# Optimization experiments

Hardware: AMD Instinct MI355X
Metric: run time of the kernel (lower is better)

Reference implementation:

```python
import jax, jax.numpy as jnp
import numpy as np

B, C, W, H, X, Y = 8, 32, 256, 128, 720, 361


def setup_inputs() -> dict:
    key = jax.random.key(0)
    k1, k2, k3, k4, k5 = jax.random.split(key, 5)
    return {
        "wt": jax.random.normal(k1, (B, C, W, H), dtype=jnp.float32),
        "x_in_lon": jax.random.uniform(k2, (B, W), dtype=jnp.float32),
        "x_in_lat": jax.random.uniform(k3, (B, H), dtype=jnp.float32),
        "x_out_lon": jax.random.uniform(k4, (B, X), dtype=jnp.float32),
        "x_out_lat": jax.random.uniform(k5, (B, Y), dtype=jnp.float32),
        "init_ls": jnp.full((1,), 0.5, dtype=jnp.float32),
    }


def _rbf_weights(x1, x2, init_ls):
    # x1: [B,N], x2: [B,M] -> RBF weights [B,N,M]
    a = x1[..., None]  # [B,N,1]
    b = x2[..., None]  # [B,M,1]
    d2 = (jnp.sum(a * a, -1)[..., :, None]
          + jnp.sum(b * b, -1)[..., None, :]
          - 2.0 * jnp.einsum('bnk,bmk->bnm', a, b))
    return jnp.exp(-0.5 * d2 / (init_ls ** 2))


def reference(wt, x_in_lon, x_in_lat, x_out_lon, x_out_lat, init_ls):
    # density channel: 1 where wt channel 0 is finite, 0 where NaN
    density = jnp.where(jnp.isnan(wt[:, 0:1]), 0.0, 1.0)
    wt = jnp.concatenate([density, wt], axis=1)          # [B,C+1,W,H]
    wt = jnp.where(jnp.isnan(wt), 0.0, wt)
    w0 = _rbf_weights(x_in_lon, x_out_lon, init_ls[0])   # [B,W,X]
    w1 = _rbf_weights(x_in_lat, x_out_lat, init_ls[0])   # [B,H,Y]
    ee = jnp.einsum('bcwh,bwx,bhy->bcxy', wt, w0, w1)    # [B,C+1,X,Y]
    dens = ee[:, 0:1]
    out = jnp.concatenate(
        [dens, ee[:, 1:] / jnp.clip(dens, 1e-6, 1e5)], axis=1)
    return out
```

## Files before the change

kernel.cpp:

```cpp
#include <hip/hip_runtime.h>

#define NB 8
#define NC 32
#define NCP 33
#define NW 256
#define NH 128
#define NX 720
#define NY 361

typedef __attribute__((ext_vector_type(8))) short  short8;
typedef __attribute__((ext_vector_type(4))) float  f32x4;

static __device__ __forceinline__ unsigned short f2bf(float f) {
    union { float f; unsigned int u; } v; v.f = f;
    unsigned int r = (v.u + 0x7FFFu + ((v.u >> 16) & 1u)) >> 16;
    return (unsigned short)r;
}

__global__ __launch_bounds__(256) void rbf_w0_kernel(
    const float* __restrict__ lon_in, const float* __restrict__ lon_out,
    const float* __restrict__ ls, unsigned short* __restrict__ w0t)
{
    int idx = blockIdx.x * 256 + threadIdx.x;
    int w = idx & (NW - 1);
    int r = idx >> 8;
    int x = r % NX;
    int b = r / NX;
    float l = ls[0];
    float inv = -0.5f / (l * l);
    float d = lon_in[b * NW + w] - lon_out[b * NX + x];
    w0t[idx] = f2bf(__expf(inv * d * d));
}

__global__ __launch_bounds__(256) void rbf_w1_kernel(
    const float* __restrict__ lat_in, const float* __restrict__ lat_out,
    const float* __restrict__ ls, unsigned short* __restrict__ w1t)
{
    int idx = blockIdx.x * 256 + threadIdx.x;
    int h = idx & (NH - 1);
    int r = idx >> 7;
    int y = r % NY;
    int b = r / NY;
    float l = ls[0];
    float inv = -0.5f / (l * l);
    float d = lat_in[b * NH + h] - lat_out[b * NY + y];
    w1t[idx] = f2bf(__expf(inv * d * d));
}

__global__ __launch_bounds__(256) void prep_wtT_kernel(
    const float* __restrict__ wt, unsigned short* __restrict__ wtT)
{
    __shared__ float tile[64 * 129];
    const int bc = blockIdx.z;
    const int b = bc / NCP;
    const int c = bc - b * NCP;
    const int w0 = blockIdx.x * 64;
    const bool dens = (c == 0);
    const float* src = wt + ((size_t)b * NC + (dens ? 0 : (c - 1))) * (NW * NH);

    const int r4 = threadIdx.x >> 5;
    const int c4 = threadIdx.x & 31;
    #pragma unroll
    for (int p = 0; p < 8; ++p) {
        int r = r4 + p * 8;
        float4 v = *(const float4*)&src[(size_t)(w0 + r) * NH + c4 * 4];
        float o0 = (v.x != v.x) ? 0.f : (dens ? 1.f : v.x);
        float o1 = (v.y != v.y) ? 0.f : (dens ? 1.f : v.y);
        float o2 = (v.z != v.z) ? 0.f : (dens ? 1.f : v.z);
        float o3 = (v.w != v.w) ? 0.f : (dens ? 1.f : v.w);
        float* tp = &tile[r * 129 + c4 * 4];
        tp[0] = o0; tp[1] = o1; tp[2] = o2; tp[3] = o3;
    }
    __syncthreads();

    unsigned short* dst = wtT + (size_t)bc * (NH * NW);
    #pragma unroll
    for (int p = 0; p < 4; ++p) {
        int ch = threadIdx.x + p * 256;
        int wc = ch & 7;
        int h  = ch >> 3;
        unsigned int u[4];
        #pragma unroll
        for (int j = 0; j < 4; ++j) {
            unsigned int lo = f2bf(tile[(wc * 8 + 2 * j    ) * 129 + h]);
            unsigned int hi = f2bf(tile[(wc * 8 + 2 * j + 1) * 129 + h]);
            u[j] = lo | (hi << 16);
        }
        uint4 q = make_uint4(u[0], u[1], u[2], u[3]);
        *(uint4*)&dst[(size_t)h * NW + w0 + wc * 8] = q;
    }
}

__global__ __launch_bounds__(256) void stage1_mfma(
    const unsigned short* __restrict__ w0t,
    const unsigned short* __restrict__ wtT,
    unsigned short* __restrict__ t)
{
    __shared__ __align__(16) unsigned short As[64 * 88];
    __shared__ __align__(16) unsigned short Bs[64 * 88];

    const int bc = blockIdx.z;
    const int b  = bc / NCP;
    const int x0 = blockIdx.x * 64;
    const int h0 = blockIdx.y * 64;
    const int tid  = threadIdx.x;
    const int lane = tid & 63;
    const int wv   = tid >> 6;
    const int q    = lane >> 4;
    const int ln   = lane & 15;
    const int mw   = (wv & 1) * 32;
    const int nw   = (wv >> 1) * 32;

    const unsigned short* Ap = w0t + (size_t)b * NX * NW;
    const unsigned short* Bp = wtT + (size_t)bc * NH * NW;

    f32x4 acc[2][2];
    #pragma unroll
    for (int i = 0; i < 2; ++i)
        #pragma unroll
        for (int j = 0; j < 2; ++j)
            acc[i][j] = (f32x4){0.f, 0.f, 0.f, 0.f};

    const int r_ld  = tid >> 3;
    const int cc_ld = tid & 7;

    for (int k0 = 0; k0 < NW; k0 += 64) {
        #pragma unroll
        for (int p = 0; p < 2; ++p) {
            int r = r_ld + p * 32;
            int xr = x0 + r; if (xr > NX - 1) xr = NX - 1;
            *(uint4*)&As[r * 88 + cc_ld * 8] =
                *(const uint4*)&Ap[(size_t)xr * NW + k0 + cc_ld * 8];
            *(uint4*)&Bs[r * 88 + cc_ld * 8] =
                *(const uint4*)&Bp[(size_t)(h0 + r) * NW + k0 + cc_ld * 8];
        }
        __syncthreads();
        #pragma unroll
        for (int ki = 0; ki < 2; ++ki) {
            const int ko = ki * 32 + q * 8;
            short8 a0 = *(const short8*)&As[(mw      + ln) * 88 + ko];
            short8 a1 = *(const short8*)&As[(mw + 16 + ln) * 88 + ko];
            short8 b0 = *(const short8*)&Bs[(nw      + ln) * 88 + ko];
            short8 b1 = *(const short8*)&Bs[(nw + 16 + ln) * 88 + ko];
            acc[0][0] = __builtin_amdgcn_mfma_f32_16x16x32_bf16(a0, b0, acc[0][0], 0, 0, 0);
            acc[0][1] = __builtin_amdgcn_mfma_f32_16x16x32_bf16(a0, b1, acc[0][1], 0, 0, 0);
            acc[1][0] = __builtin_amdgcn_mfma_f32_16x16x32_bf16(a1, b0, acc[1][0], 0, 0, 0);
            acc[1][1] = __builtin_amdgcn_mfma_f32_16x16x32_bf16(a1, b1, acc[1][1], 0, 0, 0);
        }
        __syncthreads();
    }

    unsigned short* Cp = t + (size_t)bc * NX * NH;
    #pragma unroll
    for (int mi = 0; mi < 2; ++mi)
        #pragma unroll
        for (int reg = 0; reg < 4; ++reg) {
            int x = x0 + mw + mi * 16 + q * 4 + reg;
            if (x < NX) {
                size_t rowo = (size_t)x * NH;
                #pragma unroll
                for (int ni = 0; ni < 2; ++ni) {
                    int h = h0 + nw + ni * 16 + ln;
                    Cp[rowo + h] = f2bf(acc[mi][ni][reg]);
                }
            }
        }
}

template <bool DIV>
__global__ __launch_bounds__(256) void stage2_mfma(
    const unsigned short* __restrict__ t,
    const unsigned short* __restrict__ w1t,
    float* __restrict__ out)
{
    __shared__ __align__(16) unsigned short As[64 * 88];
    __shared__ __align__(16) unsigned short Bs[64 * 88];

    int b, c;
    if (DIV) { b = blockIdx.z >> 5; c = 1 + (blockIdx.z & 31); }
    else     { b = blockIdx.z;      c = 0; }
    const int bc = b * NCP + c;
    const int x0 = blockIdx.x * 64;
    const int y0 = blockIdx.y * 64;
    const int tid  = threadIdx.x;
    const int lane = tid & 63;
    const int wv   = tid >> 6;
    const int q    = lane >> 4;
    const int ln   = lane & 15;
    const int mw   = (wv & 1) * 32;
    const int nw   = (wv >> 1) * 32;

    const unsigned short* Ap = t + (size_t)bc * NX * NH;
    const unsigned short* Bp = w1t + (size_t)b * NY * NH;

    f32x4 acc[2][2];
    #pragma unroll
    for (int i = 0; i < 2; ++i)
        #pragma unroll
        for (int j = 0; j < 2; ++j)
            acc[i][j] = (f32x4){0.f, 0.f, 0.f, 0.f};

    const int r_ld  = tid >> 3;
    const int cc_ld = tid & 7;

    for (int k0 = 0; k0 < NH; k0 += 64) {
        #pragma unroll
        for (int p = 0; p < 2; ++p) {
            int r = r_ld + p * 32;
            int xr = x0 + r; if (xr > NX - 1) xr = NX - 1;
            int yr = y0 + r; if (yr > NY - 1) yr = NY - 1;
            *(uint4*)&As[r * 88 + cc_ld * 8] =
                *(const uint4*)&Ap[(size_t)xr * NH + k0 + cc_ld * 8];
            *(uint4*)&Bs[r * 88 + cc_ld * 8] =
                *(const uint4*)&Bp[(size_t)yr * NH + k0 + cc_ld * 8];
        }
        __syncthreads();
        #pragma unroll
        for (int ki = 0; ki < 2; ++ki) {
            const int ko = ki * 32 + q * 8;
            short8 a0 = *(const short8*)&As[(mw      + ln) * 88 + ko];
            short8 a1 = *(const short8*)&As[(mw + 16 + ln) * 88 + ko];
            short8 b0 = *(const short8*)&Bs[(nw      + ln) * 88 + ko];
            short8 b1 = *(const short8*)&Bs[(nw + 16 + ln) * 88 + ko];
            acc[0][0] = __builtin_amdgcn_mfma_f32_16x16x32_bf16(a0, b0, acc[0][0], 0, 0, 0);
            acc[0][1] = __builtin_amdgcn_mfma_f32_16x16x32_bf16(a0, b1, acc[0][1], 0, 0, 0);
            acc[1][0] = __builtin_amdgcn_mfma_f32_16x16x32_bf16(a1, b0, acc[1][0], 0, 0, 0);
            acc[1][1] = __builtin_amdgcn_mfma_f32_16x16x32_bf16(a1, b1, acc[1][1], 0, 0, 0);
        }
        __syncthreads();
    }

    const size_t plane = (size_t)NX * NY;
    float* Cp = out + (size_t)bc * plane;
    const float* Dp = out + (size_t)(b * NCP) * plane;

    #pragma unroll
    for (int mi = 0; mi < 2; ++mi)
        #pragma unroll
        for (int reg = 0; reg < 4; ++reg) {
            int x = x0 + mw + mi * 16 + q * 4 + reg;
            if (x < NX) {
                size_t rowo = (size_t)x * NY;
                #pragma unroll
                for (int ni = 0; ni < 2; ++ni) {
                    int y = y0 + nw + ni * 16 + ln;
                    if (y < NY) {
                        float val = acc[mi][ni][reg];
                        if (DIV) {
                            float dv = Dp[rowo + y];
                            dv = fminf(fmaxf(dv, 1e-6f), 1e5f);
                            val /= dv;
                        }
                        Cp[rowo + y] = val;
                    }
                }
            }
        }
}

extern "C" void kernel_launch(void* const* d_in, const int* in_sizes, int n_in,
                              void* d_out, int out_size, void* d_ws, size_t ws_size,
                              hipStream_t stream)
{
    const float* wt      = (const float*)d_in[0];
    const float* lon_in  = (const float*)d_in[1];
    const float* lat_in  = (const float*)d_in[2];
    const float* lon_out = (const float*)d_in[3];
    const float* lat_out = (const float*)d_in[4];
    const float* ls      = (const float*)d_in[5];
    float* out = (float*)d_out;

    unsigned short* w0t = (unsigned short*)d_ws;
    unsigned short* w1t = w0t + (size_t)NB * NX * NW;
    unsigned short* wtT = w1t + (size_t)NB * NY * NH;
    unsigned short* t   = wtT + (size_t)NB * NCP * NH * NW;

    rbf_w0_kernel<<<(NB * NX * NW) / 256, 256, 0, stream>>>(lon_in, lon_out, ls, w0t);
    rbf_w1_kernel<<<(NB * NY * NH) / 256, 256, 0, stream>>>(lat_in, lat_out, ls, w1t);

    dim3 g3(4, 1, NB * NCP);
    prep_wtT_kernel<<<g3, 256, 0, stream>>>(wt, wtT);

    dim3 g1(12, 2, NB * NCP);
    stage1_mfma<<<g1, 256, 0, stream>>>(w0t, wtT, t);

    dim3 g2a(12, 6, NB);
    stage2_mfma<false><<<g2a, 256, 0, stream>>>(t, w1t, out);

    dim3 g2b(12, 6, NB * NC);
    stage2_mfma<true><<<g2b, 256, 0, stream>>>(t, w1t, out);
}
```

Before: 465.4 us.

## Fuse both contraction stages into one kernel keeping the intermediate in LDS

Stage 1 (w0 contraction) and stage 2 (w1 contraction plus density division) are merged into one kernel per (x-tile, batch, channel). Each block computes a 64x128 bf16 intermediate tile into shared memory, then loops over all y tiles to produce the output. This removes the global write and re-read of the intermediate tensor and one kernel launch. In exchange, the density pass launches only 96 blocks, and each block runs its y loop serially, which lowers parallelism per launch.

```diff
diff --git a/kernel.cpp b/kernel.cpp
--- a/kernel.cpp
+++ b/kernel.cpp
@@ -91,171 +91,153 @@
     }
 }
 
-__global__ __launch_bounds__(256) void stage1_mfma(
+template <bool DIV>
+__global__ __launch_bounds__(256) void fused_stage(
     const unsigned short* __restrict__ w0t,
     const unsigned short* __restrict__ wtT,
-    unsigned short* __restrict__ t)
-{
-    __shared__ __align__(16) unsigned short As[64 * 88];
-    __shared__ __align__(16) unsigned short Bs[64 * 88];
-
-    const int bc = blockIdx.z;
-    const int b  = bc / NCP;
+    const unsigned short* __restrict__ w1t,
+    float* __restrict__ out)
+{
+    __shared__ __align__(16) unsigned short T[64 * 136];
+    __shared__ __align__(16) unsigned short S[64 * 72 + 128 * 72];
+
+    int b, c;
+    if (DIV) { b = blockIdx.y >> 5; c = 1 + (blockIdx.y & 31); }
+    else     { b = blockIdx.y;      c = 0; }
+    const int bc = b * NCP + c;
     const int x0 = blockIdx.x * 64;
-    const int h0 = blockIdx.y * 64;
+
     const int tid  = threadIdx.x;
     const int lane = tid & 63;
     const int wv   = tid >> 6;
     const int q    = lane >> 4;
     const int ln   = lane & 15;
-    const int mw   = (wv & 1) * 32;
-    const int nw   = (wv >> 1) * 32;
 
     const unsigned short* Ap = w0t + (size_t)b * NX * NW;
     const unsigned short* Bp = wtT + (size_t)bc * NH * NW;
-
-    f32x4 acc[2][2];
+    const unsigned short* Vp = w1t + (size_t)b * NY * NH;
+
+    unsigned short* As = S;
+    unsigned short* Bs = S + 64 * 72;
+
+    const int mw1 = (wv & 1) * 32;
+    const int nh1 = (wv >> 1) * 64;
+
+    f32x4 acc1[2][4];
     #pragma unroll
     for (int i = 0; i < 2; ++i)
         #pragma unroll
-        for (int j = 0; j < 2; ++j)
-            acc[i][j] = (f32x4){0.f, 0.f, 0.f, 0.f};
-
-    const int r_ld  = tid >> 3;
-    const int cc_ld = tid & 7;
+        for (int j = 0; j < 4; ++j)
+            acc1[i][j] = (f32x4){0.f, 0.f, 0.f, 0.f};
+
+    const int ar  = tid >> 2;
+    const int ac  = (tid & 3) * 16;
+    int xr = x0 + ar; if (xr > NX - 1) xr = NX - 1;
+    const int brr = tid >> 1;
+    const int bcc = (tid & 1) * 32;
 
     for (int k0 = 0; k0 < NW; k0 += 64) {
-        #pragma unroll
-        for (int p = 0; p < 2; ++p) {
-            int r = r_ld + p * 32;
-            int xr = x0 + r; if (xr > NX - 1) xr = NX - 1;
-            *(uint4*)&As[r * 88 + cc_ld * 8] =
-                *(const uint4*)&Ap[(size_t)xr * NW + k0 + cc_ld * 8];
-            *(uint4*)&Bs[r * 88 + cc_ld * 8] =
-                *(const uint4*)&Bp[(size_t)(h0 + r) * NW + k0 + cc_ld * 8];
-        }
+        const unsigned short* Arow = Ap + (size_t)xr * NW + k0 + ac;
+        *(uint4*)&As[ar * 72 + ac    ] = *(const uint4*)&Arow[0];
+        *(uint4*)&As[ar * 72 + ac + 8] = *(const uint4*)&Arow[8];
+        const unsigned short* Brow = Bp + (size_t)brr * NW + k0 + bcc;
+        #pragma unroll
+        for (int j = 0; j < 4; ++j)
+            *(uint4*)&Bs[brr * 72 + bcc + j * 8] = *(const uint4*)&Brow[j * 8];
         __syncthreads();
         #pragma unroll
         for (int ki = 0; ki < 2; ++ki) {
             const int ko = ki * 32 + q * 8;
-            short8 a0 = *(const short8*)&As[(mw      + ln) * 88 + ko];
-            short8 a1 = *(const short8*)&As[(mw + 16 + ln) * 88 + ko];
-            short8 b0 = *(const short8*)&Bs[(nw      + ln) * 88 + ko];
-            short8 b1 = *(const short8*)&Bs[(nw + 16 + ln) * 88 + ko];
+            short8 a0 = *(const short8*)&As[(mw1      + ln) * 72 + ko];
+            short8 a1 = *(const short8*)&As[(mw1 + 16 + ln) * 72 + ko];
+            #pragma unroll
+            for (int nn = 0; nn < 4; ++nn) {
+                short8 bb = *(const short8*)&Bs[(nh1 + nn * 16 + ln) * 72 + ko];
+                acc1[0][nn] = __builtin_amdgcn_mfma_f32_16x16x32_bf16(a0, bb, acc1[0][nn], 0, 0, 0);
+                acc1[1][nn] = __builtin_amdgcn_mfma_f32_16x16x32_bf16(a1, bb, acc1[1][nn], 0, 0, 0);
+            }
+        }
+        __syncthreads();
+    }
+
+    #pragma unroll
+    for (int nn = 0; nn < 4; ++nn) {
+        const int col = nh1 + nn * 16 + ln;
+        #pragma unroll
+        for (int mi = 0; mi < 2; ++mi) {
+            #pragma unroll
+            for (int reg = 0; reg < 4; ++reg) {
+                int row = mw1 + mi * 16 + q * 4 + reg;
+                T[row * 136 + col] = f2bf(acc1[mi][nn][reg]);
+            }
+        }
+    }
+    __syncthreads();
+
+    unsigned short* Bs2 = S;
+    const int mw2 = (wv & 1) * 32;
+    const int nw2 = (wv >> 1) * 32;
+
+    const size_t plane = (size_t)NX * NY;
+    float* Cp = out + (size_t)bc * plane;
+    const float* Dp = out + (size_t)(b * NCP) * plane;
+
+    const int vr = tid >> 2;
+    const int vc = (tid & 3) * 32;
+
+    for (int y0 = 0; y0 < 384; y0 += 64) {
+        int yy = y0 + vr; if (yy > NY - 1) yy = NY - 1;
+        const unsigned short* Vrow = Vp + (size_t)yy * NH + vc;
+        #pragma unroll
+        for (int j = 0; j < 4; ++j)
+            *(uint4*)&Bs2[vr * 136 + vc + j * 8] = *(const uint4*)&Vrow[j * 8];
+        __syncthreads();
+
+        f32x4 acc[2][2];
+        #pragma unroll
+        for (int i = 0; i < 2; ++i)
+            #pragma unroll
+            for (int j = 0; j < 2; ++j)
+                acc[i][j] = (f32x4){0.f, 0.f, 0.f, 0.f};
+
+        #pragma unroll
+        for (int ki = 0; ki < 4; ++ki) {
+            const int ko = ki * 32 + q * 8;
+            short8 a0 = *(const short8*)&T[(mw2      + ln) * 136 + ko];
+            short8 a1 = *(const short8*)&T[(mw2 + 16 + ln) * 136 + ko];
+            short8 b0 = *(const short8*)&Bs2[(nw2      + ln) * 136 + ko];
+            short8 b1 = *(const short8*)&Bs2[(nw2 + 16 + ln) * 136 + ko];
             acc[0][0] = __builtin_amdgcn_mfma_f32_16x16x32_bf16(a0, b0, acc[0][0], 0, 0, 0);
             acc[0][1] = __builtin_amdgcn_mfma_f32_16x16x32_bf16(a0, b1, acc[0][1], 0, 0, 0);
             acc[1][0] = __builtin_amdgcn_mfma_f32_16x16x32_bf16(a1, b0, acc[1][0], 0, 0, 0);
             acc[1][1] = __builtin_amdgcn_mfma_f32_16x16x32_bf16(a1, b1, acc[1][1], 0, 0, 0);
         }
         __syncthreads();
-    }
-
-    unsigned short* Cp = t + (size_t)bc * NX * NH;
-    #pragma unroll
-    for (int mi = 0; mi < 2; ++mi)
-        #pragma unroll
-        for (int reg = 0; reg < 4; ++reg) {
-            int x = x0 + mw + mi * 16 + q * 4 + reg;
-            if (x < NX) {
-                size_t rowo = (size_t)x * NH;
-                #pragma unroll
-                for (int ni = 0; ni < 2; ++ni) {
-                    int h = h0 + nw + ni * 16 + ln;
-                    Cp[rowo + h] = f2bf(acc[mi][ni][reg]);
-                }
-            }
-        }
-}
-
-template <bool DIV>
-__global__ __launch_bounds__(256) void stage2_mfma(
-    const unsigned short* __restrict__ t,
-    const unsigned short* __restrict__ w1t,
-    float* __restrict__ out)
-{
-    __shared__ __align__(16) unsigned short As[64 * 88];
-    __shared__ __align__(16) unsigned short Bs[64 * 88];
-
-    int b, c;
-    if (DIV) { b = blockIdx.z >> 5; c = 1 + (blockIdx.z & 31); }
-    else     { b = blockIdx.z;      c = 0; }
-    const int bc = b * NCP + c;
-    const int x0 = blockIdx.x * 64;
-    const int y0 = blockIdx.y * 64;
-    const int tid  = threadIdx.x;
-    const int lane = tid & 63;
-    const int wv   = tid >> 6;
-    const int q    = lane >> 4;
-    const int ln   = lane & 15;
-    const int mw   = (wv & 1) * 32;
-    const int nw   = (wv >> 1) * 32;
-
-    const unsigned short* Ap = t + (size_t)bc * NX * NH;
-    const unsigned short* Bp = w1t + (size_t)b * NY * NH;
-
-    f32x4 acc[2][2];
-    #pragma unroll
-    for (int i = 0; i < 2; ++i)
-        #pragma unroll
-        for (int j = 0; j < 2; ++j)
-            acc[i][j] = (f32x4){0.f, 0.f, 0.f, 0.f};
-
-    const int r_ld  = tid >> 3;
-    const int cc_ld = tid & 7;
-
-    for (int k0 = 0; k0 < NH; k0 += 64) {
-        #pragma unroll
-        for (int p = 0; p < 2; ++p) {
-            int r = r_ld + p * 32;
-            int xr = x0 + r; if (xr > NX - 1) xr = NX - 1;
-            int yr = y0 + r; if (yr > NY - 1) yr = NY - 1;
-            *(uint4*)&As[r * 88 + cc_ld * 8] =
-                *(const uint4*)&Ap[(size_t)xr * NH + k0 + cc_ld * 8];
-            *(uint4*)&Bs[r * 88 + cc_ld * 8] =
-                *(const uint4*)&Bp[(size_t)yr * NH + k0 + cc_ld * 8];
-        }
-        __syncthreads();
-        #pragma unroll
-        for (int ki = 0; ki < 2; ++ki) {
-            const int ko = ki * 32 + q * 8;
-            short8 a0 = *(const short8*)&As[(mw      + ln) * 88 + ko];
-            short8 a1 = *(const short8*)&As[(mw + 16 + ln) * 88 + ko];
-            short8 b0 = *(const short8*)&Bs[(nw      + ln) * 88 + ko];
-            short8 b1 = *(const short8*)&Bs[(nw + 16 + ln) * 88 + ko];
-            acc[0][0] = __builtin_amdgcn_mfma_f32_16x16x32_bf16(a0, b0, acc[0][0], 0, 0, 0);
-            acc[0][1] = __builtin_amdgcn_mfma_f32_16x16x32_bf16(a0, b1, acc[0][1], 0, 0, 0);
-            acc[1][0] = __builtin_amdgcn_mfma_f32_16x16x32_bf16(a1, b0, acc[1][0], 0, 0, 0);
-            acc[1][1] = __builtin_amdgcn_mfma_f32_16x16x32_bf16(a1, b1, acc[1][1], 0, 0, 0);
-        }
-        __syncthreads();
-    }
-
-    const size_t plane = (size_t)NX * NY;
-    float* Cp = out + (size_t)bc * plane;
-    const float* Dp = out + (size_t)(b * NCP) * plane;
-
-    #pragma unroll
-    for (int mi = 0; mi < 2; ++mi)
-        #pragma unroll
-        for (int reg = 0; reg < 4; ++reg) {
-            int x = x0 + mw + mi * 16 + q * 4 + reg;
-            if (x < NX) {
-                size_t rowo = (size_t)x * NY;
-                #pragma unroll
-                for (int ni = 0; ni < 2; ++ni) {
-                    int y = y0 + nw + ni * 16 + ln;
-                    if (y < NY) {
-                        float val = acc[mi][ni][reg];
-                        if (DIV) {
-                            float dv = Dp[rowo + y];
-                            dv = fminf(fmaxf(dv, 1e-6f), 1e5f);
-                            val /= dv;
+
+        #pragma unroll
+        for (int mi = 0; mi < 2; ++mi) {
+            #pragma unroll
+            for (int reg = 0; reg < 4; ++reg) {
+                int x = x0 + mw2 + mi * 16 + q * 4 + reg;
+                if (x < NX) {
+                    size_t rowo = (size_t)x * NY;
+                    #pragma unroll
+                    for (int nj = 0; nj < 2; ++nj) {
+                        int y = y0 + nw2 + nj * 16 + ln;
+                        if (y < NY) {
+                            float val = acc[mi][nj][reg];
+                            if (DIV) {
+                                float dv = Dp[rowo + y];
+                                dv = fminf(fmaxf(dv, 1e-6f), 1e5f);
+                                val /= dv;
+                            }
+                            Cp[rowo + y] = val;
                         }
-                        Cp[rowo + y] = val;
                     }
                 }
             }
         }
+    }
 }
 
 extern "C" void kernel_launch(void* const* d_in, const int* in_sizes, int n_in,
@@ -273,7 +255,6 @@
     unsigned short* w0t = (unsigned short*)d_ws;
     unsigned short* w1t = w0t + (size_t)NB * NX * NW;
     unsigned short* wtT = w1t + (size_t)NB * NY * NH;
-    unsigned short* t   = wtT + (size_t)NB * NCP * NH * NW;
 
     rbf_w0_kernel<<<(NB * NX * NW) / 256, 256, 0, stream>>>(lon_in, lon_out, ls, w0t);
     rbf_w1_kernel<<<(NB * NY * NH) / 256, 256, 0, stream>>>(lat_in, lat_out, ls, w1t);
@@ -281,12 +262,9 @@
     dim3 g3(4, 1, NB * NCP);
     prep_wtT_kernel<<<g3, 256, 0, stream>>>(wt, wtT);
 
-    dim3 g1(12, 2, NB * NCP);
-    stage1_mfma<<<g1, 256, 0, stream>>>(w0t, wtT, t);
-
-    dim3 g2a(12, 6, NB);
-    stage2_mfma<false><<<g2a, 256, 0, stream>>>(t, w1t, out);
-
-    dim3 g2b(12, 6, NB * NC);
-    stage2_mfma<true><<<g2b, 256, 0, stream>>>(t, w1t, out);
-}
+    dim3 gd(12, NB);
+    fused_stage<false><<<gd, 256, 0, stream>>>(w0t, wtT, w1t, out);
+
+    dim3 gm(12, NB * NC);
+    fused_stage<true><<<gm, 256, 0, stream>>>(w0t, wtT, w1t, out);
+}
```

Measured after the change: 514.1 us. 1.1x slower.
